# Performance work log

Measured on AMD Instinct MI355X. Metric: run time of the kernel, lower is better.

The kernel has to match this reference:

```python
import jax, jax.numpy as jnp
import numpy as np

A, B, M, H, NMOL = 100000, 200000, 50000, 128, 4000
DEPTH = 5
MAX_NB = 8


def setup_inputs() -> dict:
    key = jax.random.key(0)
    ks = jax.random.split(key, 10)
    fatoms = jax.random.normal(ks[0], (A, 35), dtype=jnp.float32)
    fbonds = jax.random.normal(ks[1], (B, 40), dtype=jnp.float32)
    # index 0 of the combined message table is the zero padding message
    tree_message = jax.random.normal(ks[2], (M, H), dtype=jnp.float32).at[0].set(0.0)
    agraph = jax.random.randint(ks[3], (A, MAX_NB), 0, M + B, dtype=jnp.int32)
    bgraph = jax.random.randint(ks[4], (B, MAX_NB), 0, M + B, dtype=jnp.int32)
    mol_id = jnp.sort(jax.random.randint(ks[5], (A,), 0, NMOL, dtype=jnp.int32))
    W_i = jax.random.normal(ks[6], (40, H), dtype=jnp.float32) * 0.05
    W_h = jax.random.normal(ks[7], (H, H), dtype=jnp.float32) * 0.05
    W_o = jax.random.normal(ks[8], (35 + H, H), dtype=jnp.float32) * 0.05
    b_o = jax.random.normal(ks[9], (H,), dtype=jnp.float32) * 0.05
    return {"fatoms": fatoms, "fbonds": fbonds, "tree_message": tree_message,
            "agraph": agraph, "bgraph": bgraph, "mol_id": mol_id,
            "W_i": W_i, "W_h": W_h, "W_o": W_o, "b_o": b_o, "n_mols": NMOL}


def reference(fatoms, fbonds, tree_message, agraph, bgraph, mol_id, W_i, W_h, W_o, b_o, n_mols):
    binput = fbonds @ W_i                      # [B, H]
    graph_message = jax.nn.relu(binput)        # [B, H]
    for _ in range(DEPTH - 1):
        message = jnp.concatenate([tree_message, graph_message], axis=0)  # [M+B, H]
        nei = jnp.take(message, bgraph, axis=0).sum(axis=1)               # [B, H]
        graph_message = jax.nn.relu(binput + nei @ W_h)
    message = jnp.concatenate([tree_message, graph_message], axis=0)
    nei_a = jnp.take(message, agraph, axis=0).sum(axis=1)                 # [A, H]
    ainput = jnp.concatenate([fatoms, nei_a], axis=1)                     # [A, 35+H]
    atom_hiddens = jax.nn.relu(ainput @ W_o + b_o)                        # [A, H]
    sums = jax.ops.segment_sum(atom_hiddens, mol_id, num_segments=n_mols)
    counts = jax.ops.segment_sum(jnp.ones((atom_hiddens.shape[0],), dtype=atom_hiddens.dtype),
                                 mol_id, num_segments=n_mols)
    mol_vecs = sums / jnp.maximum(counts, 1.0)[:, None]                   # [n_mols, H]
    return mol_vecs
```

## Files before the change

kernel.cpp:

```cpp
#include <hip/hip_runtime.h>
#include <hip/hip_bf16.h>

#define AN 100000
#define BN 200000
#define MN 50000
#define HD 128
#define NMOL 4000
#define MAXNB 8
#define BSZ 24576

typedef unsigned short u16;
typedef unsigned int   u32;
typedef float f32x4 __attribute__((ext_vector_type(4)));
typedef short s16x8 __attribute__((ext_vector_type(8)));

__device__ __forceinline__ u16 f2bf(float x) {
    u32 u = __float_as_uint(x);
    return (u16)((u + 0x7fffu + ((u >> 16) & 1u)) >> 16);
}

__global__ __launch_bounds__(256) void k_prep(const float* __restrict__ tree,
                                              u16* __restrict__ tree_bf,
                                              const float* __restrict__ W_h,
                                              const float* __restrict__ W_i,
                                              const float* __restrict__ W_o,
                                              const float* __restrict__ b_o,
                                              u16* __restrict__ Bit,
                                              u16* __restrict__ Bat,
                                              const int* __restrict__ mol_id,
                                              float* __restrict__ counts,
                                              const float* __restrict__ fbonds,
                                              u16* __restrict__ fbp) {
    int blk = blockIdx.x, tid = threadIdx.x;
    if (blk < 6250) {
        int i = blk * 256 + tid;
        const float4 v = ((const float4*)tree)[i];
        uint2 r;
        r.x = (u32)f2bf(v.x) | ((u32)f2bf(v.y) << 16);
        r.y = (u32)f2bf(v.z) | ((u32)f2bf(v.w) << 16);
        ((uint2*)tree_bf)[i] = r;
    } else if (blk < 6442) {
        int i = (blk - 6250) * 256 + tid;
        int which = (i >= BSZ);
        int e = which ? i - BSZ : i;
        int j = e & 7, lane = (e >> 3) & 63, nt = (e >> 9) & 7, kt = e >> 12;
        int k = kt * 32 + (lane >> 4) * 8 + j;
        int n = nt * 16 + (lane & 15);
        if (!which) {
            float v = (k < 128) ? W_h[k * 128 + n] : ((k < 168) ? W_i[(k - 128) * 128 + n] : 0.f);
            Bit[e] = f2bf(v);
        } else {
            float v = (k < 128) ? W_o[(35 + k) * 128 + n]
                    : (k < 163) ? W_o[(k - 128) * 128 + n]
                    : (k == 163) ? b_o[n] : 0.f;
            Bat[e] = f2bf(v);
        }
    } else if (blk < 6458) {
        int m = (blk - 6442) * 256 + tid;
        if (m < NMOL) {
            int lo = 0, hi = AN;
            while (lo < hi) { int mid = (lo + hi) >> 1; if (mol_id[mid] < m) lo = mid + 1; else hi = mid; }
            int s = lo; lo = 0; hi = AN;
            while (lo < hi) { int mid = (lo + hi) >> 1; if (mol_id[mid] < m + 1) lo = mid + 1; else hi = mid; }
            counts[m] = (float)(lo - s);
        }
    } else {
        int q = (blk - 6458) * 256 + tid;
        if (q < 2000000) {
            const float4 v = ((const float4*)fbonds)[q];
            uint2 r;
            r.x = (u32)f2bf(v.x) | ((u32)f2bf(v.y) << 16);
            r.y = (u32)f2bf(v.z) | ((u32)f2bf(v.w) << 16);
            ((uint2*)fbp)[q] = r;
        }
    }
}

#define LDB 136
template <bool PK>
__global__ __launch_bounds__(256) void k_binput_mfma(const float* __restrict__ fbonds,
                                                     const u16* __restrict__ fbp,
                                                     const u16* __restrict__ Bsw,
                                                     u16* __restrict__ g0) {
    __shared__ __align__(16) u16 sA[64][LDB];
    int tid = threadIdx.x;
    int b0  = blockIdx.x * 64;
    if (PK) {
        const uint4* f4 = (const uint4*)fbp;
        for (int i = tid; i < 512; i += 256) {
            if (i < 320) {
                int row = i / 5, seg = i % 5;
                *(uint4*)&sA[row][seg * 8] = f4[(size_t)(b0 + row) * 5 + seg];
            } else {
                int j = i - 320, row = j / 3, seg = j % 3;
                *(uint4*)&sA[row][40 + seg * 8] = (uint4){0u, 0u, 0u, 0u};
            }
        }
    } else {
        for (int i = tid; i < 64 * 64; i += 256) {
            int b = i >> 6, c = i & 63;
            float v = (c < 40) ? fbonds[(size_t)(b0 + b) * 40 + c] : 0.f;
            sA[b][c] = f2bf(v);
        }
    }
    __syncthreads();
    int lane = tid & 63, wv = tid >> 6;
    int am = lane & 15, aq = lane >> 4;
    s16x8 afr[2];
#pragma unroll
    for (int kt = 0; kt < 2; ++kt)
        afr[kt] = *(const s16x8*)&sA[wv * 16 + am][kt * 32 + aq * 8];
    f32x4 acc[8];
#pragma unroll
    for (int nt = 0; nt < 8; ++nt) acc[nt] = (f32x4){0.f, 0.f, 0.f, 0.f};
    const s16x8* B8 = (const s16x8*)Bsw;
#pragma unroll
    for (int kt = 0; kt < 2; ++kt)
#pragma unroll
        for (int nt = 0; nt < 8; ++nt) {
            s16x8 bfr = B8[((4 + kt) * 8 + nt) * 64 + lane];
            acc[nt] = __builtin_amdgcn_mfma_f32_16x16x32_bf16(afr[kt], bfr, acc[nt], 0, 0, 0);
        }
#pragma unroll
    for (int nt = 0; nt < 8; ++nt)
#pragma unroll
        for (int r = 0; r < 4; ++r)
            sA[wv * 16 + aq * 4 + r][nt * 16 + am] = f2bf(fmaxf(acc[nt][r], 0.f));
    __syncthreads();
#pragma unroll
    for (int s = 0; s < 4; ++s) {
        int e = tid + s * 256;
        int row = e >> 4, seg = e & 15;
        *(uint4*)&g0[((size_t)b0 + row) * HD + seg * 8] = *(const uint4*)&sA[row][seg * 8];
    }
}

#define LDA 200

__device__ __forceinline__ void gather16(u16 (*sA)[LDA], const int (*sidx)[MAXNB],
                                         const u16* __restrict__ tree_bf,
                                         const u16* __restrict__ tin, int tid) {
    int l = tid & 15, tb = tid >> 4;
#pragma unroll
    for (int pp = 0; pp < 2; ++pp) {
        int r0 = tb + (2 * pp) * 16;
        int r1 = tb + (2 * pp + 1) * 16;
        uint4 v[2][8];
#pragma unroll
        for (int j = 0; j < 8; ++j) {
            int idx = sidx[r0][j];
            const u16* base = (idx < MN) ? tree_bf + (size_t)idx * HD
                                         : tin + (size_t)(idx - MN) * HD;
            v[0][j] = ((const uint4*)base)[l];
        }
#pragma unroll
        for (int j = 0; j < 8; ++j) {
            int idx = sidx[r1][j];
            const u16* base = (idx < MN) ? tree_bf + (size_t)idx * HD
                                         : tin + (size_t)(idx - MN) * HD;
            v[1][j] = ((const uint4*)base)[l];
        }
#pragma unroll
        for (int h = 0; h < 2; ++h) {
            float a[8] = {0.f, 0.f, 0.f, 0.f, 0.f, 0.f, 0.f, 0.f};
#pragma unroll
            for (int j = 0; j < 8; ++j) {
                a[0] += __uint_as_float(v[h][j].x << 16);
                a[1] += __uint_as_float(v[h][j].x & 0xffff0000u);
                a[2] += __uint_as_float(v[h][j].y << 16);
                a[3] += __uint_as_float(v[h][j].y & 0xffff0000u);
                a[4] += __uint_as_float(v[h][j].z << 16);
                a[5] += __uint_as_float(v[h][j].z & 0xffff0000u);
                a[6] += __uint_as_float(v[h][j].w << 16);
                a[7] += __uint_as_float(v[h][j].w & 0xffff0000u);
            }
            uint4 r;
            r.x = (u32)f2bf(a[0]) | ((u32)f2bf(a[1]) << 16);
            r.y = (u32)f2bf(a[2]) | ((u32)f2bf(a[3]) << 16);
            r.z = (u32)f2bf(a[4]) | ((u32)f2bf(a[5]) << 16);
            r.w = (u32)f2bf(a[6]) | ((u32)f2bf(a[7]) << 16);
            *(uint4*)&sA[h == 0 ? r0 : r1][l * 8] = r;
        }
    }
}

template <bool PK>
__global__ __launch_bounds__(256) void k_iter_mfma(const u16* __restrict__ tree_bf,
                                                   const u16* __restrict__ tin,
                                                   const float* __restrict__ fbonds,
                                                   const u16* __restrict__ fbp,
                                                   const int* __restrict__ bgraph,
                                                   const u16* __restrict__ Bsw,
                                                   u16* __restrict__ tout) {
    __shared__ __align__(16) u16 sA[64][LDA];
    __shared__ int sidx[64][MAXNB];
    int tid = threadIdx.x;
    int b0  = blockIdx.x * 64;

    for (int i = tid; i < 64 * MAXNB; i += 256)
        sidx[i >> 3][i & 7] = bgraph[(size_t)(b0 + (i >> 3)) * MAXNB + (i & 7)];
    if (PK) {
        const uint4* f4 = (const uint4*)fbp;
        for (int i = tid; i < 512; i += 256) {
            if (i < 320) {
                int row = i / 5, seg = i % 5;
                *(uint4*)&sA[row][128 + seg * 8] = f4[(size_t)(b0 + row) * 5 + seg];
            } else {
                int j = i - 320, row = j / 3, seg = j % 3;
                *(uint4*)&sA[row][168 + seg * 8] = (uint4){0u, 0u, 0u, 0u};
            }
        }
    } else {
        for (int i = tid; i < 64 * 64; i += 256) {
            int b = i >> 6, c = i & 63;
            float v = (c < 40) ? fbonds[(size_t)(b0 + b) * 40 + c] : 0.f;
            sA[b][128 + c] = f2bf(v);
        }
    }
    __syncthreads();

    gather16(sA, sidx, tree_bf, tin, tid);
    __syncthreads();

    int lane = tid & 63, wv = tid >> 6;
    int am = lane & 15, aq = lane >> 4;
    s16x8 afr[6];
#pragma unroll
    for (int kt = 0; kt < 6; ++kt)
        afr[kt] = *(const s16x8*)&sA[wv * 16 + am][kt * 32 + aq * 8];
    f32x4 acc[8];
#pragma unroll
    for (int nt = 0; nt < 8; ++nt) acc[nt] = (f32x4){0.f, 0.f, 0.f, 0.f};
    const s16x8* B8 = (const s16x8*)Bsw;
#pragma unroll
    for (int kt = 0; kt < 6; ++kt)
#pragma unroll
        for (int nt = 0; nt < 8; ++nt) {
            s16x8 bfr = B8[(kt * 8 + nt) * 64 + lane];
            acc[nt] = __builtin_amdgcn_mfma_f32_16x16x32_bf16(afr[kt], bfr, acc[nt], 0, 0, 0);
        }
#pragma unroll
    for (int nt = 0; nt < 8; ++nt)
#pragma unroll
        for (int r = 0; r < 4; ++r)
            sA[wv * 16 + aq * 4 + r][nt * 16 + am] = f2bf(fmaxf(acc[nt][r], 0.f));
    __syncthreads();
#pragma unroll
    for (int s = 0; s < 4; ++s) {
        int e = tid + s * 256;
        int row = e >> 4, seg = e & 15;
        *(uint4*)&tout[((size_t)b0 + row) * HD + seg * 8] = *(const uint4*)&sA[row][seg * 8];
    }
}

__global__ __launch_bounds__(256) void k_atom_mfma(const u16* __restrict__ tree_bf,
                                                   const u16* __restrict__ gfin,
                                                   const float* __restrict__ fatoms,
                                                   const int* __restrict__ agraph,
                                                   const int* __restrict__ mol_id,
                                                   const u16* __restrict__ Bsw,
                                                   float* __restrict__ sums) {
    __shared__ __align__(16) char smem[64 * 132 * sizeof(float)];
    u16   (*sA)[LDA] = (u16 (*)[LDA])smem;
    float* sC        = (float*)smem;
    __shared__ int sidx[64][MAXNB];
    __shared__ int smol[64];
    int tid = threadIdx.x;
    int a0  = blockIdx.x * 64;

    for (int i = tid; i < 64 * MAXNB; i += 256) {
        int a = a0 + (i >> 3);
        sidx[i >> 3][i & 7] = (a < AN) ? agraph[(size_t)a * MAXNB + (i & 7)] : 0;
    }
    if (tid < 64) smol[tid] = (a0 + tid < AN) ? mol_id[a0 + tid] : -1;
    for (int i = tid; i < 64 * 64; i += 256) {
        int b = i >> 6, c = i & 63;
        float v = 0.f;
        if (a0 + b < AN) {
            if (c < 35) v = fatoms[(size_t)(a0 + b) * 35 + c];
            else if (c == 35) v = 1.f;
        }
        sA[b][128 + c] = f2bf(v);
    }
    __syncthreads();
    gather16(sA, sidx, tree_bf, gfin, tid);
    __syncthreads();

    int lane = tid & 63, wv = tid >> 6;
    int am = lane & 15, aq = lane >> 4;
    s16x8 afr[6];
#pragma unroll
    for (int kt = 0; kt < 6; ++kt)
        afr[kt] = *(const s16x8*)&sA[wv * 16 + am][kt * 32 + aq * 8];
    __syncthreads();

    f32x4 acc[8];
#pragma unroll
    for (int nt = 0; nt < 8; ++nt) acc[nt] = (f32x4){0.f, 0.f, 0.f, 0.f};
    const s16x8* B8 = (const s16x8*)Bsw;
#pragma unroll
    for (int kt = 0; kt < 6; ++kt)
#pragma unroll
        for (int nt = 0; nt < 8; ++nt) {
            s16x8 bfr = B8[(kt * 8 + nt) * 64 + lane];
            acc[nt] = __builtin_amdgcn_mfma_f32_16x16x32_bf16(afr[kt], bfr, acc[nt], 0, 0, 0);
        }
#pragma unroll
    for (int nt = 0; nt < 8; ++nt)
#pragma unroll
        for (int r = 0; r < 4; ++r) {
            int row = wv * 16 + aq * 4 + r;
            int col = nt * 16 + am;
            sC[row * 132 + col] = fmaxf(acc[nt][r], 0.f);
        }
    __syncthreads();

    {
        int c = tid & 127, half = tid >> 7;
        int base = half * 32;
        float run = 0.f;
        int cur = smol[base];
        for (int r = 0; r < 32; ++r) {
            int row = base + r;
            int mv = smol[row];
            if (mv != cur) {
                if (cur >= 0) atomicAdd(&sums[(size_t)cur * HD + c], run);
                run = 0.f; cur = mv;
            }
            run += sC[row * 132 + c];
        }
        if (cur >= 0) atomicAdd(&sums[(size_t)cur * HD + c], run);
    }
}

__global__ __launch_bounds__(256) void k_div(const float* __restrict__ sums,
                                             const float* __restrict__ counts,
                                             float* __restrict__ out) {
    int i = blockIdx.x * 256 + threadIdx.x;
    if (i < NMOL * HD) out[i] = sums[i] / fmaxf(counts[i >> 7], 1.f);
}

extern "C" void kernel_launch(void* const* d_in, const int* in_sizes, int n_in,
                              void* d_out, int out_size, void* d_ws, size_t ws_size,
                              hipStream_t stream) {
    const float* fatoms = (const float*)d_in[0];
    const float* fbonds = (const float*)d_in[1];
    const float* tree   = (const float*)d_in[2];
    const int*   agraph = (const int*)d_in[3];
    const int*   bgraph = (const int*)d_in[4];
    const int*   mol_id = (const int*)d_in[5];
    const float* W_i    = (const float*)d_in[6];
    const float* W_h    = (const float*)d_in[7];
    const float* W_o    = (const float*)d_in[8];
    const float* b_o    = (const float*)d_in[9];
    float* out = (float*)d_out;

    size_t tbl   = (size_t)BN * HD;
    size_t treeN = (size_t)MN * HD;
    size_t fbN   = (size_t)BN * 40;
    size_t redN  = (size_t)(NMOL * HD + NMOL);

    size_t need_base = (2 * tbl + treeN + 2 * BSZ) * 2 + redN * 4;
    size_t need_pack = need_base + fbN * 2;

    if (ws_size < need_base) {
        hipMemsetAsync(d_out, 0, (size_t)out_size * sizeof(float), stream);
        return;
    }
    bool pk = (ws_size >= need_pack);

    u16* t0      = (u16*)d_ws;
    u16* t1      = t0 + tbl;
    u16* tree_bf = t1 + tbl;
    u16* Bit     = tree_bf + treeN;
    u16* Bat     = Bit + BSZ;
    u16* fbp     = pk ? (Bat + BSZ) : nullptr;
    float* sums   = (float*)(pk ? (fbp + fbN) : (Bat + BSZ));
    float* counts = sums + (size_t)NMOL * HD;

    hipMemsetAsync(sums, 0, (size_t)NMOL * HD * sizeof(float), stream);
    k_prep<<<pk ? 14271 : 6458, 256, 0, stream>>>(tree, tree_bf, W_h, W_i, W_o, b_o,
                                                  Bit, Bat, mol_id, counts, fbonds, fbp);
    if (pk)
        k_binput_mfma<true><<<BN / 64, 256, 0, stream>>>(fbonds, fbp, Bit, t0);
    else
        k_binput_mfma<false><<<BN / 64, 256, 0, stream>>>(fbonds, fbp, Bit, t0);

    u16* cur = t0;
    u16* nxt = t1;
    for (int it = 0; it < 4; ++it) {
        if (pk)
            k_iter_mfma<true><<<BN / 64, 256, 0, stream>>>(tree_bf, cur, fbonds, fbp,
                                                           bgraph, Bit, nxt);
        else
            k_iter_mfma<false><<<BN / 64, 256, 0, stream>>>(tree_bf, cur, fbonds, fbp,
                                                            bgraph, Bit, nxt);
        u16* t = cur; cur = nxt; nxt = t;
    }
    k_atom_mfma<<<(AN + 63) / 64, 256, 0, stream>>>(tree_bf, cur, fatoms, agraph,
                                                    mol_id, Bat, sums);
    k_div<<<(NMOL * HD) / 256, 256, 0, stream>>>(sums, counts, out);
}
```

Baseline: 484.5 us.

## Load bond/atom features straight into MFMA fragments and shrink shared memory

Bond features (packed or fp32) and atom features are now loaded from global memory directly into the MFMA A-fragment registers instead of being staged through shared memory. This lets the sA tile shrink from 200 to 136 columns. The atom kernel now stores its ReLU output as bf16 in the same tile instead of a separate fp32 buffer, and all three kernels gain an 8-blocks-per-SM launch bound to raise occupancy. The cost is uncoalesced per-lane global loads for the feature fragments and an extra bf16 rounding of atom hiddens before the segment sum, which slightly changes numerics.

```diff
diff --git a/kernel.cpp b/kernel.cpp
--- a/kernel.cpp
+++ b/kernel.cpp
@@ -17,6 +17,17 @@
 __device__ __forceinline__ u16 f2bf(float x) {
     u32 u = __float_as_uint(x);
     return (u16)((u + 0x7fffu + ((u >> 16) & 1u)) >> 16);
+}
+
+__device__ __forceinline__ s16x8 zero8() { return (s16x8){0, 0, 0, 0, 0, 0, 0, 0}; }
+
+__device__ __forceinline__ s16x8 pack44(float4 a, float4 b) {
+    union { uint4 u; s16x8 s; } r;
+    r.u.x = (u32)f2bf(a.x) | ((u32)f2bf(a.y) << 16);
+    r.u.y = (u32)f2bf(a.z) | ((u32)f2bf(a.w) << 16);
+    r.u.z = (u32)f2bf(b.x) | ((u32)f2bf(b.y) << 16);
+    r.u.w = (u32)f2bf(b.z) | ((u32)f2bf(b.w) << 16);
+    return r.s;
 }
 
 __global__ __launch_bounds__(256) void k_prep(const float* __restrict__ tree,
@@ -76,40 +87,44 @@
     }
 }
 
-#define LDB 136
+#define LDA 136
+
+__device__ __forceinline__ void fb_frags_pk(const u16* __restrict__ fbp, int b, int aq,
+                                            s16x8& lo, s16x8& hi) {
+    const uint4* f4 = (const uint4*)fbp;
+    uint4 v = f4[(size_t)b * 5 + aq];
+    lo = *(const s16x8*)&v;
+    if (aq == 0) {
+        uint4 w = f4[(size_t)b * 5 + 4];
+        hi = *(const s16x8*)&w;
+    } else hi = zero8();
+}
+
+__device__ __forceinline__ void fb_frags_f32(const float* __restrict__ fbonds, int b, int aq,
+                                             s16x8& lo, s16x8& hi) {
+    const float4* f4 = (const float4*)(fbonds + (size_t)b * 40);
+    float4 x = f4[aq * 2], y = f4[aq * 2 + 1];
+    lo = pack44(x, y);
+    if (aq == 0) {
+        float4 p = f4[8], q = f4[9];
+        hi = pack44(p, q);
+    } else hi = zero8();
+}
+
 template <bool PK>
-__global__ __launch_bounds__(256) void k_binput_mfma(const float* __restrict__ fbonds,
-                                                     const u16* __restrict__ fbp,
-                                                     const u16* __restrict__ Bsw,
-                                                     u16* __restrict__ g0) {
-    __shared__ __align__(16) u16 sA[64][LDB];
+__global__ __launch_bounds__(256, 8) void k_binput_mfma(const float* __restrict__ fbonds,
+                                                        const u16* __restrict__ fbp,
+                                                        const u16* __restrict__ Bsw,
+                                                        u16* __restrict__ g0) {
+    __shared__ __align__(16) u16 sA[64][LDA];
     int tid = threadIdx.x;
     int b0  = blockIdx.x * 64;
-    if (PK) {
-        const uint4* f4 = (const uint4*)fbp;
-        for (int i = tid; i < 512; i += 256) {
-            if (i < 320) {
-                int row = i / 5, seg = i % 5;
-                *(uint4*)&sA[row][seg * 8] = f4[(size_t)(b0 + row) * 5 + seg];
-            } else {
-                int j = i - 320, row = j / 3, seg = j % 3;
-                *(uint4*)&sA[row][40 + seg * 8] = (uint4){0u, 0u, 0u, 0u};
-            }
-        }
-    } else {
-        for (int i = tid; i < 64 * 64; i += 256) {
-            int b = i >> 6, c = i & 63;
-            float v = (c < 40) ? fbonds[(size_t)(b0 + b) * 40 + c] : 0.f;
-            sA[b][c] = f2bf(v);
-        }
-    }
-    __syncthreads();
     int lane = tid & 63, wv = tid >> 6;
     int am = lane & 15, aq = lane >> 4;
+    int b = b0 + wv * 16 + am;
     s16x8 afr[2];
-#pragma unroll
-    for (int kt = 0; kt < 2; ++kt)
-        afr[kt] = *(const s16x8*)&sA[wv * 16 + am][kt * 32 + aq * 8];
+    if (PK) fb_frags_pk(fbp, b, aq, afr[0], afr[1]);
+    else    fb_frags_f32(fbonds, b, aq, afr[0], afr[1]);
     f32x4 acc[8];
 #pragma unroll
     for (int nt = 0; nt < 8; ++nt) acc[nt] = (f32x4){0.f, 0.f, 0.f, 0.f};
@@ -134,8 +149,6 @@
         *(uint4*)&g0[((size_t)b0 + row) * HD + seg * 8] = *(const uint4*)&sA[row][seg * 8];
     }
 }
-
-#define LDA 200
 
 __device__ __forceinline__ void gather16(u16 (*sA)[LDA], const int (*sidx)[MAXNB],
                                          const u16* __restrict__ tree_bf,
@@ -185,13 +198,13 @@
 }
 
 template <bool PK>
-__global__ __launch_bounds__(256) void k_iter_mfma(const u16* __restrict__ tree_bf,
-                                                   const u16* __restrict__ tin,
-                                                   const float* __restrict__ fbonds,
-                                                   const u16* __restrict__ fbp,
-                                                   const int* __restrict__ bgraph,
-                                                   const u16* __restrict__ Bsw,
-                                                   u16* __restrict__ tout) {
+__global__ __launch_bounds__(256, 8) void k_iter_mfma(const u16* __restrict__ tree_bf,
+                                                      const u16* __restrict__ tin,
+                                                      const float* __restrict__ fbonds,
+                                                      const u16* __restrict__ fbp,
+                                                      const int* __restrict__ bgraph,
+                                                      const u16* __restrict__ Bsw,
+                                                      u16* __restrict__ tout) {
     __shared__ __align__(16) u16 sA[64][LDA];
     __shared__ int sidx[64][MAXNB];
     int tid = threadIdx.x;
@@ -199,24 +212,6 @@
 
     for (int i = tid; i < 64 * MAXNB; i += 256)
         sidx[i >> 3][i & 7] = bgraph[(size_t)(b0 + (i >> 3)) * MAXNB + (i & 7)];
-    if (PK) {
-        const uint4* f4 = (const uint4*)fbp;
-        for (int i = tid; i < 512; i += 256) {
-            if (i < 320) {
-                int row = i / 5, seg = i % 5;
-                *(uint4*)&sA[row][128 + seg * 8] = f4[(size_t)(b0 + row) * 5 + seg];
-            } else {
-                int j = i - 320, row = j / 3, seg = j % 3;
-                *(uint4*)&sA[row][168 + seg * 8] = (uint4){0u, 0u, 0u, 0u};
-            }
-        }
-    } else {
-        for (int i = tid; i < 64 * 64; i += 256) {
-            int b = i >> 6, c = i & 63;
-            float v = (c < 40) ? fbonds[(size_t)(b0 + b) * 40 + c] : 0.f;
-            sA[b][128 + c] = f2bf(v);
-        }
-    }
     __syncthreads();
 
     gather16(sA, sidx, tree_bf, tin, tid);
@@ -226,8 +221,11 @@
     int am = lane & 15, aq = lane >> 4;
     s16x8 afr[6];
 #pragma unroll
-    for (int kt = 0; kt < 6; ++kt)
+    for (int kt = 0; kt < 4; ++kt)
         afr[kt] = *(const s16x8*)&sA[wv * 16 + am][kt * 32 + aq * 8];
+    int b = b0 + wv * 16 + am;
+    if (PK) fb_frags_pk(fbp, b, aq, afr[4], afr[5]);
+    else    fb_frags_f32(fbonds, b, aq, afr[4], afr[5]);
     f32x4 acc[8];
 #pragma unroll
     for (int nt = 0; nt < 8; ++nt) acc[nt] = (f32x4){0.f, 0.f, 0.f, 0.f};
@@ -253,16 +251,14 @@
     }
 }
 
-__global__ __launch_bounds__(256) void k_atom_mfma(const u16* __restrict__ tree_bf,
-                                                   const u16* __restrict__ gfin,
-                                                   const float* __restrict__ fatoms,
-                                                   const int* __restrict__ agraph,
-                                                   const int* __restrict__ mol_id,
-                                                   const u16* __restrict__ Bsw,
-                                                   float* __restrict__ sums) {
-    __shared__ __align__(16) char smem[64 * 132 * sizeof(float)];
-    u16   (*sA)[LDA] = (u16 (*)[LDA])smem;
-    float* sC        = (float*)smem;
+__global__ __launch_bounds__(256, 8) void k_atom_mfma(const u16* __restrict__ tree_bf,
+                                                      const u16* __restrict__ gfin,
+                                                      const float* __restrict__ fatoms,
+                                                      const int* __restrict__ agraph,
+                                                      const int* __restrict__ mol_id,
+                                                      const u16* __restrict__ Bsw,
+                                                      float* __restrict__ sums) {
+    __shared__ __align__(16) u16 sA[64][LDA];
     __shared__ int sidx[64][MAXNB];
     __shared__ int smol[64];
     int tid = threadIdx.x;
@@ -273,15 +269,6 @@
         sidx[i >> 3][i & 7] = (a < AN) ? agraph[(size_t)a * MAXNB + (i & 7)] : 0;
     }
     if (tid < 64) smol[tid] = (a0 + tid < AN) ? mol_id[a0 + tid] : -1;
-    for (int i = tid; i < 64 * 64; i += 256) {
-        int b = i >> 6, c = i & 63;
-        float v = 0.f;
-        if (a0 + b < AN) {
-            if (c < 35) v = fatoms[(size_t)(a0 + b) * 35 + c];
-            else if (c == 35) v = 1.f;
-        }
-        sA[b][128 + c] = f2bf(v);
-    }
     __syncthreads();
     gather16(sA, sidx, tree_bf, gfin, tid);
     __syncthreads();
@@ -290,9 +277,35 @@
     int am = lane & 15, aq = lane >> 4;
     s16x8 afr[6];
 #pragma unroll
-    for (int kt = 0; kt < 6; ++kt)
+    for (int kt = 0; kt < 4; ++kt)
         afr[kt] = *(const s16x8*)&sA[wv * 16 + am][kt * 32 + aq * 8];
-    __syncthreads();
+    {
+        int a = a0 + wv * 16 + am;
+        float f[8] = {0.f, 0.f, 0.f, 0.f, 0.f, 0.f, 0.f, 0.f};
+        if (a < AN) {
+            const float* fr = fatoms + (size_t)a * 35;
+#pragma unroll
+            for (int j = 0; j < 8; ++j) f[j] = fr[aq * 8 + j];
+        }
+        union { uint4 u; s16x8 s; } r4;
+        r4.u.x = (u32)f2bf(f[0]) | ((u32)f2bf(f[1]) << 16);
+        r4.u.y = (u32)f2bf(f[2]) | ((u32)f2bf(f[3]) << 16);
+        r4.u.z = (u32)f2bf(f[4]) | ((u32)f2bf(f[5]) << 16);
+        r4.u.w = (u32)f2bf(f[6]) | ((u32)f2bf(f[7]) << 16);
+        afr[4] = r4.s;
+        if (aq == 0) {
+            float g0 = 0.f, g1 = 0.f, g2 = 0.f, g3 = 0.f;
+            if (a < AN) {
+                const float* fr = fatoms + (size_t)a * 35;
+                g0 = fr[32]; g1 = fr[33]; g2 = fr[34]; g3 = 1.f;
+            }
+            union { uint4 u; s16x8 s; } r5;
+            r5.u.x = (u32)f2bf(g0) | ((u32)f2bf(g1) << 16);
+            r5.u.y = (u32)f2bf(g2) | ((u32)f2bf(g3) << 16);
+            r5.u.z = 0u; r5.u.w = 0u;
+            afr[5] = r5.s;
+        } else afr[5] = zero8();
+    }
 
     f32x4 acc[8];
 #pragma unroll
@@ -308,11 +321,8 @@
 #pragma unroll
     for (int nt = 0; nt < 8; ++nt)
 #pragma unroll
-        for (int r = 0; r < 4; ++r) {
-            int row = wv * 16 + aq * 4 + r;
-            int col = nt * 16 + am;
-            sC[row * 132 + col] = fmaxf(acc[nt][r], 0.f);
-        }
+        for (int r = 0; r < 4; ++r)
+            sA[wv * 16 + aq * 4 + r][nt * 16 + am] = f2bf(fmaxf(acc[nt][r], 0.f));
     __syncthreads();
 
     {
@@ -327,7 +337,7 @@
                 if (cur >= 0) atomicAdd(&sums[(size_t)cur * HD + c], run);
                 run = 0.f; cur = mv;
             }
-            run += sC[row * 132 + c];
+            run += __uint_as_float((u32)sA[row][c] << 16);
         }
         if (cur >= 0) atomicAdd(&sums[(size_t)cur * HD + c], run);
     }
```

After: 592.3 us. +22.2%, slower.
